# Performance work log

Measured on AMD Instinct MI355X. Metric: run time of the kernel, lower is better.

The kernel has to match this reference:

```python
import jax, jax.numpy as jnp
import numpy as np

KROT = 8        # number of pairwise-rotation layers (hard-coded in Rotation)
GROUP = 128     # rotation group size (hard-coded)
QGS = 128       # quantization group size (hard-coded in RotateLinearAWQMarlinInt4)


def setup_inputs() -> dict:
    rng = np.random.default_rng(0)
    M, K, N = 32, 8192, 28672
    G = K // QGS  # 64 quant groups
    shifts = np.arange(8, dtype=np.uint32) * 4
    # activations
    x = jnp.asarray(rng.standard_normal((M, K)), dtype=jnp.float16)
    # int4 weights packed 8-per-int32 along the out dim (nibble j of word n -> column n*8+j)
    nib = rng.integers(0, 16, size=(K, N // 8, 8), dtype=np.uint32)
    qweight = jnp.asarray((nib << shifts).sum(-1, dtype=np.uint32).view(np.int32))  # (K, N//8)
    znib = rng.integers(0, 16, size=(G, N // 8, 8), dtype=np.uint32)
    qzeros = jnp.asarray((znib << shifts).sum(-1, dtype=np.uint32).view(np.int32))  # (G, N//8)
    scales = jnp.asarray(rng.uniform(0.001, 0.01, (G, N)), dtype=jnp.float16)
    bias = jnp.asarray(rng.standard_normal(N) * 0.01, dtype=jnp.float16)
    # rotation params: per-layer angles over all K//2 pairs; one local permutation of
    # 0..127 per layer, shared across all K//GROUP groups (as in Rotation.__init__)
    theta = jnp.asarray(rng.uniform(-0.2, 0.2, (KROT, K // 2)), dtype=jnp.float16)
    pairs = jnp.asarray(np.stack([rng.permutation(GROUP) for _ in range(KROT)]).astype(np.int32))  # (KROT, 128)
    channel_scales = jnp.asarray(rng.uniform(0.5, 2.0, (1, K)), dtype=jnp.float16)
    return dict(x=x, qweight=qweight, qzeros=qzeros, scales=scales, bias=bias,
                theta=theta, pairs=pairs, channel_scales=channel_scales)


def _rotate(x, pairs, theta, channel_scales):
    # x: (M, K). Apply KROT layers of Givens rotations on channel pairs within each
    # 128-wide group, then per-channel scaling.
    M, K = x.shape
    ng = K // GROUP
    xg = x.reshape(M, ng, GROUP)
    for k in range(KROT):
        p = pairs[k]                      # (128,) local permutation
        i, j = p[0::2], p[1::2]           # (64,) disjoint index sets
        th = theta[k].reshape(ng, GROUP // 2).astype(jnp.float32)  # (ng, 64) per-group angles
        c = jnp.cos(th).astype(x.dtype)
        s = jnp.sin(th).astype(x.dtype)
        xi = xg[:, :, i]
        xj = xg[:, :, j]
        xg = xg.at[:, :, i].set(c * xi - s * xj)
        xg = xg.at[:, :, j].set(s * xi + c * xj)
    return xg.reshape(M, K) * channel_scales


def _dequant(qweight, qzeros, scales):
    # unpack 8 uint4 nibbles per int32 along the out dim; dequant per quant group
    K = qweight.shape[0]
    shifts = jnp.arange(8, dtype=jnp.int32) * 4
    w = ((qweight[:, :, None] >> shifts) & 0xF).reshape(K, -1)       # (K, N) ints 0..15
    z = ((qzeros[:, :, None] >> shifts) & 0xF).reshape(qzeros.shape[0], -1)  # (G, N)
    zf = jnp.repeat(z.astype(scales.dtype), QGS, axis=0)             # (K, N)
    sf = jnp.repeat(scales, QGS, axis=0)                             # (K, N)
    return (w.astype(scales.dtype) - zf) * sf


def reference(x, qweight, qzeros, scales, bias, theta, pairs, channel_scales):
    xr = _rotate(x, pairs, theta, channel_scales)   # (M, K)
    W = _dequant(qweight, qzeros, scales)           # (K, N)
    return xr @ W + bias
```

## Files before the change

kernel.cpp:

```cpp
#include <hip/hip_runtime.h>
#include <hip/hip_bf16.h>

using uint32   = unsigned int;
using ushort_t = unsigned short;
using short8   = __attribute__((ext_vector_type(8))) short;
using uint4v   = __attribute__((ext_vector_type(4))) uint32;
using float4v  = __attribute__((ext_vector_type(4))) float;
using floatx16 = __attribute__((ext_vector_type(16))) float;

#define M_DIM 32
#define K_DIM 8192
#define N_DIM 28672
#define QROW  (N_DIM/8)
#define KSPLIT 8
#define BN    256
#define CH    128
#define NCH   8
#define TSTRIDE 132

__device__ ushort_t g_xr2[M_DIM * K_DIM];
__device__ float    g_S[64 * M_DIM];

__device__ __forceinline__ float bf2f(ushort_t u){
  unsigned int v = ((unsigned int)u) << 16;
  return __builtin_bit_cast(float, v);
}
__device__ __forceinline__ ushort_t f2bf(float f){
  return __builtin_bit_cast(ushort_t, __float2bfloat16(f));
}

__global__ __launch_bounds__(256) void rotate_kernel(
    const float* __restrict__ x, const float* __restrict__ theta,
    const int* __restrict__ pairs, const float* __restrict__ cs)
{
  __shared__ float xb[4][128];
  const int u    = threadIdx.x >> 6;
  const int lane = threadIdx.x & 63;
  const int id   = blockIdx.x * 4 + u;
  const int m    = id >> 6;
  const int g    = id & 63;
  const float* xp = x + m*K_DIM + g*128;
  int   ip[8], jp[8];
  float cv[8], sv[8];
  #pragma unroll
  for (int k = 0; k < 8; ++k){
    ip[k] = pairs[k*128 + 2*lane];
    jp[k] = pairs[k*128 + 2*lane + 1];
    const float th = theta[k*(K_DIM/2) + g*64 + lane];
    cv[k] = cosf(th); sv[k] = sinf(th);
  }
  xb[u][lane]    = xp[lane];
  xb[u][lane+64] = xp[lane+64];
  #pragma unroll
  for (int k = 0; k < 8; ++k){
    __syncthreads();
    const float xi = xb[u][ip[k]], xj = xb[u][jp[k]];
    xb[u][ip[k]] = cv[k]*xi - sv[k]*xj;
    xb[u][jp[k]] = sv[k]*xi + cv[k]*xj;
  }
  __syncthreads();
  const int base = g*128;
  const int k0 = base + lane, k1 = base + lane + 64;
  const ushort_t b0 = f2bf(xb[u][lane]    * cs[k0]);
  const ushort_t b1 = f2bf(xb[u][lane+64] * cs[k1]);
  g_xr2[(((size_t)(k0>>3))*32 + m)*8 + (k0&7)] = b0;
  g_xr2[(((size_t)(k1>>3))*32 + m)*8 + (k1&7)] = b1;
  float sum = bf2f(b0) + bf2f(b1);
  #pragma unroll
  for (int d = 32; d > 0; d >>= 1) sum += __shfl_xor(sum, d, 64);
  if (lane == 0) g_S[g*M_DIM + m] = sum;
}

__global__ __launch_bounds__(256) void bias_kernel(
    const float* __restrict__ bias, float* __restrict__ out)
{
  const int n  = (blockIdx.x % (N_DIM/256))*256 + threadIdx.x;
  const int m0 = (blockIdx.x / (N_DIM/256))*8;
  const float b = bias[n];
  #pragma unroll
  for (int m = 0; m < 8; ++m) out[(size_t)(m0+m)*N_DIM + n] = b;
}

__global__ __launch_bounds__(512, 4) void gemm_kernel(
    const uint32* __restrict__ qw, const uint32* __restrict__ qz,
    const float* __restrict__ scales, float* __restrict__ out)
{
  __shared__ uint32 T[8 * 2 * 4 * TSTRIDE];
  const int bid  = blockIdx.x;
  const int ks   = bid & 7;
  const int nb   = bid >> 3;
  const int tid  = threadIdx.x;
  const int w    = tid >> 6;
  const int lane = tid & 63;
  const int l31  = lane & 31;
  const int koct = lane >> 5;
  const int n0   = nb * BN;
  const int n    = n0 + w*32 + l31;
  const uint32 sh = (uint32)((l31 & 7)*4);
  const int colr = l31 >> 3;
  const int k0   = ks * (NCH*CH);

  uint32* Tw = &T[w * (2*4*TSTRIDE)];

  const uint32* bbase = qw + (size_t)k0*QROW + (n0>>3) + w*4;
  const ushort_t* abase = g_xr2 + (size_t)k0*32;

  float accT[16];
  #pragma unroll
  for (int r = 0; r < 16; ++r) accT[r] = 0.f;

  uint4v bva[2], bvb[2];
  bva[0] = *(const uint4v*)(bbase + (size_t)lane*QROW);
  bvb[0] = *(const uint4v*)(bbase + (size_t)(lane+64)*QROW);

  #pragma unroll 2
  for (int c = 0; c < NCH; ++c){
    const int cb = c & 1, nx = cb ^ 1;
    uint32* Tc = Tw + cb*(4*TSTRIDE);
    #pragma unroll
    for (int j = 0; j < 4; ++j){
      Tc[j*TSTRIDE + lane]      = bva[cb][j];
      Tc[j*TSTRIDE + lane + 64] = bvb[cb][j];
    }
    if (c + 1 < NCH){
      const uint32* bb = bbase + (size_t)(c+1)*CH*QROW;
      bva[nx] = *(const uint4v*)(bb + (size_t)lane*QROW);
      bvb[nx] = *(const uint4v*)(bb + (size_t)(lane+64)*QROW);
    }
    const float  s  = scales[(size_t)(ks*NCH + c)*N_DIM + n];
    const uint32 zq = qz[(size_t)(ks*NCH + c)*QROW + (n>>3)];
    const ushort_t* ab = abase + (size_t)c*CH*32;

    floatx16 acc;
    #pragma unroll
    for (int r = 0; r < 16; ++r) acc[r] = 0.f;

    #pragma unroll
    for (int kh = 0; kh < 2; ++kh){
      short8 av[4];
      #pragma unroll
      for (int i = 0; i < 4; ++i){
        const int kk = kh*4 + i;
        av[i] = *(const short8*)(ab + ((kk*2 + koct)*32 + l31)*8);
      }
      #pragma unroll
      for (int i = 0; i < 4; ++i){
        const int kk = kh*4 + i;
        const uint32* tp = Tc + colr*TSTRIDE + kk*16 + koct*8;
        const uint4v p0 = *(const uint4v*)(tp);
        const uint4v p1 = *(const uint4v*)(tp + 4);
        uint4v bp;
        bp.x = ((p0.x >> sh) & 15u) | (((p0.y >> sh) & 15u) << 16) | 0x43004300u;
        bp.y = ((p0.z >> sh) & 15u) | (((p0.w >> sh) & 15u) << 16) | 0x43004300u;
        bp.z = ((p1.x >> sh) & 15u) | (((p1.y >> sh) & 15u) << 16) | 0x43004300u;
        bp.w = ((p1.z >> sh) & 15u) | (((p1.w >> sh) & 15u) << 16) | 0x43004300u;
        acc = __builtin_amdgcn_mfma_f32_32x32x16_bf16(
                  av[i], __builtin_bit_cast(short8, bp), acc, 0, 0, 0);
      }
    }
    const float t = s * (float)(128u + ((zq >> sh) & 15u));
    const float* Sg = &g_S[(size_t)(ks*NCH + c)*M_DIM];
    float4v Sv[4];
    #pragma unroll
    for (int q = 0; q < 4; ++q)
      Sv[q] = *(const float4v*)(Sg + q*8 + 4*koct);
    #pragma unroll
    for (int r = 0; r < 16; ++r){
      accT[r] = fmaf(s, acc[r], accT[r]);
      accT[r] = fmaf(-t, Sv[r >> 2][r & 3], accT[r]);
    }
  }
  #pragma unroll
  for (int r = 0; r < 16; ++r){
    const int row = (r & 3) + 8*(r >> 2) + 4*koct;
    atomicAdd(out + (size_t)row*N_DIM + n, accT[r]);
  }
}

extern "C" void kernel_launch(void* const* d_in, const int* in_sizes, int n_in,
                              void* d_out, int out_size, void* d_ws, size_t ws_size,
                              hipStream_t stream)
{
  const float*  x      = (const float*)d_in[0];
  const uint32* qw     = (const uint32*)d_in[1];
  const uint32* qz     = (const uint32*)d_in[2];
  const float*  scales = (const float*)d_in[3];
  const float*  bias   = (const float*)d_in[4];
  const float*  theta  = (const float*)d_in[5];
  const int*    pairs  = (const int*)d_in[6];
  const float*  cs     = (const float*)d_in[7];
  float* out = (float*)d_out;

  rotate_kernel<<<dim3((M_DIM*64)/4), dim3(256), 0, stream>>>(x, theta, pairs, cs);
  bias_kernel<<<dim3((N_DIM/256)*4), dim3(256), 0, stream>>>(bias, out);
  gemm_kernel<<<dim3((N_DIM/BN)*KSPLIT), dim3(512), 0, stream>>>(qw, qz, scales, out);
}
```

Before: 255.8 us.

## Load weight tiles cooperatively across block with shared double buffer and doubled K-split

```diff
diff --git a/kernel.cpp b/kernel.cpp
--- a/kernel.cpp
+++ b/kernel.cpp
@@ -12,10 +12,10 @@
 #define K_DIM 8192
 #define N_DIM 28672
 #define QROW  (N_DIM/8)
-#define KSPLIT 8
+#define KSPLIT 16
 #define BN    256
 #define CH    128
-#define NCH   8
+#define NCH   4
 #define TSTRIDE 132
 
 __device__ ushort_t g_xr2[M_DIM * K_DIM];
@@ -85,10 +85,10 @@
     const uint32* __restrict__ qw, const uint32* __restrict__ qz,
     const float* __restrict__ scales, float* __restrict__ out)
 {
-  __shared__ uint32 T[8 * 2 * 4 * TSTRIDE];
+  __shared__ uint32 T[2][32*TSTRIDE];
   const int bid  = blockIdx.x;
-  const int ks   = bid & 7;
-  const int nb   = bid >> 3;
+  const int ks   = bid & (KSPLIT-1);
+  const int nb   = bid >> 4;
   const int tid  = threadIdx.x;
   const int w    = tid >> 6;
   const int lane = tid & 63;
@@ -97,36 +97,47 @@
   const int n0   = nb * BN;
   const int n    = n0 + w*32 + l31;
   const uint32 sh = (uint32)((l31 & 7)*4);
-  const int colr = l31 >> 3;
+  const int col  = w*4 + (l31 >> 3);
   const int k0   = ks * (NCH*CH);
 
-  uint32* Tw = &T[w * (2*4*TSTRIDE)];
-
-  const uint32* bbase = qw + (size_t)k0*QROW + (n0>>3) + w*4;
+  const int brow = tid >> 3;
+  const int bcq  = tid & 7;
+  const uint32* bbase = qw + (size_t)(k0 + brow)*QROW + (n0>>3) + bcq*4;
   const ushort_t* abase = g_xr2 + (size_t)k0*32;
 
   float accT[16];
   #pragma unroll
   for (int r = 0; r < 16; ++r) accT[r] = 0.f;
 
-  uint4v bva[2], bvb[2];
-  bva[0] = *(const uint4v*)(bbase + (size_t)lane*QROW);
-  bvb[0] = *(const uint4v*)(bbase + (size_t)(lane+64)*QROW);
-
-  #pragma unroll 2
+  uint4v bv0[2], bv1[2];
+
+  bv0[0] = *(const uint4v*)(bbase);
+  bv1[0] = *(const uint4v*)(bbase + (size_t)64*QROW);
+  #pragma unroll
+  for (int j = 0; j < 4; ++j){
+    T[0][(bcq*4 + j)*TSTRIDE + brow]      = bv0[0][j];
+    T[0][(bcq*4 + j)*TSTRIDE + brow + 64] = bv1[0][j];
+  }
+  bv0[1] = *(const uint4v*)(bbase + (size_t)CH*QROW);
+  bv1[1] = *(const uint4v*)(bbase + (size_t)CH*QROW + (size_t)64*QROW);
+  __syncthreads();
+
+  #pragma unroll
   for (int c = 0; c < NCH; ++c){
     const int cb = c & 1, nx = cb ^ 1;
-    uint32* Tc = Tw + cb*(4*TSTRIDE);
-    #pragma unroll
-    for (int j = 0; j < 4; ++j){
-      Tc[j*TSTRIDE + lane]      = bva[cb][j];
-      Tc[j*TSTRIDE + lane + 64] = bvb[cb][j];
+    if (c + 2 < NCH){
+      const uint32* bb = bbase + (size_t)(c+2)*CH*QROW;
+      bv0[cb] = *(const uint4v*)(bb);
+      bv1[cb] = *(const uint4v*)(bb + (size_t)64*QROW);
     }
     if (c + 1 < NCH){
-      const uint32* bb = bbase + (size_t)(c+1)*CH*QROW;
-      bva[nx] = *(const uint4v*)(bb + (size_t)lane*QROW);
-      bvb[nx] = *(const uint4v*)(bb + (size_t)(lane+64)*QROW);
-    }
+      #pragma unroll
+      for (int j = 0; j < 4; ++j){
+        T[nx][(bcq*4 + j)*TSTRIDE + brow]      = bv0[nx][j];
+        T[nx][(bcq*4 + j)*TSTRIDE + brow + 64] = bv1[nx][j];
+      }
+    }
+
     const float  s  = scales[(size_t)(ks*NCH + c)*N_DIM + n];
     const uint32 zq = qz[(size_t)(ks*NCH + c)*QROW + (n>>3)];
     const ushort_t* ab = abase + (size_t)c*CH*32;
@@ -146,7 +157,7 @@
       #pragma unroll
       for (int i = 0; i < 4; ++i){
         const int kk = kh*4 + i;
-        const uint32* tp = Tc + colr*TSTRIDE + kk*16 + koct*8;
+        const uint32* tp = &T[cb][col*TSTRIDE + kk*16 + koct*8];
         const uint4v p0 = *(const uint4v*)(tp);
         const uint4v p1 = *(const uint4v*)(tp + 4);
         uint4v bp;
@@ -169,6 +180,7 @@
       accT[r] = fmaf(s, acc[r], accT[r]);
       accT[r] = fmaf(-t, Sv[r >> 2][r & 3], accT[r]);
     }
+    if (c + 1 < NCH) __syncthreads();
   }
   #pragma unroll
   for (int r = 0; r < 16; ++r){
```

After: 231.5 us. 9.5% less time.
